# Kernel optimization log

Measured on AMD Instinct MI355X. Metric: run time of the kernel, lower is better.

Reference implementation:

```python
import jax, jax.numpy as jnp
import numpy as np

C = 256          # in_channels == out_channels
L = 131072       # sequence length (multiple of BL)
BL = 64          # dilation == sliding-attention block length
CQ = C // 2      # q/k channels (r1=2)
CV = C // 2      # v channels (r2=2)
ALPHA = 1.0
EPS_IN = 1e-5    # InstanceNorm eps


def setup_inputs() -> dict:
    key = jax.random.key(0)
    ks = jax.random.split(key, 16)
    s = 0.05
    return {
        "x": jax.random.normal(ks[0], (1, C, L), jnp.float32),
        "f": jax.random.normal(ks[1], (1, C, L), jnp.float32),
        "mask": jnp.ones((1, 1, L), jnp.float32),
        # ConvFeedForward: Conv1d(C, C, 3, padding=BL, dilation=BL)
        "Wff": jax.random.normal(ks[2], (C, C, 3), jnp.float32) * s,
        "bff": jax.random.normal(ks[3], (C,), jnp.float32) * s,
        # AttLayer 1x1 convs
        "Wq": jax.random.normal(ks[4], (CQ, C), jnp.float32) * s,
        "bq": jax.random.normal(ks[5], (CQ,), jnp.float32) * s,
        "Wk": jax.random.normal(ks[6], (CQ, C), jnp.float32) * s,
        "bk": jax.random.normal(ks[7], (CQ,), jnp.float32) * s,
        "Wv": jax.random.normal(ks[8], (CV, C), jnp.float32) * s,
        "bv": jax.random.normal(ks[9], (CV,), jnp.float32) * s,
        "Wo": jax.random.normal(ks[10], (C, CV), jnp.float32) * s,
        "bo": jax.random.normal(ks[11], (C,), jnp.float32) * s,
        # AttModule.conv_1x1
        "Wc": jax.random.normal(ks[12], (C, C), jnp.float32) * s,
        "bc": jax.random.normal(ks[13], (C,), jnp.float32) * s,
    }


def _conv1x1(W, b, x):  # x: (B, Cin, L)
    return jnp.einsum('oc,bcl->bol', W, x) + b[None, :, None]


def _forward(x, f, mask, Wff, bff, Wq, bq, Wk, bk, Wv, bv, Wo, bo, Wc, bc):
    # --- ConvFeedForward: dilated conv + ReLU (same-length output) ---
    out = jax.lax.conv_general_dilated(
        x, Wff, window_strides=(1,), padding=[(BL, BL)], rhs_dilation=(BL,),
        dimension_numbers=('NCH', 'OIH', 'NCH')) + bff[None, :, None]
    out = jax.nn.relu(out)  # (1, C, L)

    # --- InstanceNorm1d (affine=False, biased var) ---
    mu = out.mean(axis=-1, keepdims=True)
    var = out.var(axis=-1, keepdims=True)
    xn = (out - mu) * jax.lax.rsqrt(var + EPS_IN)

    # --- AttLayer (sliding_att, decoder: value from f) ---
    q = _conv1x1(Wq, bq, xn)   # (1, CQ, L)
    k = _conv1x1(Wk, bk, xn)   # (1, CQ, L)
    v = _conv1x1(Wv, bv, f)    # (1, CV, L)

    nb = L // BL
    half = BL // 2
    pm = mask[:, 0:1, :]                         # (1,1,L) padding mask
    # pad halo of BL//2 zeros on each side of k, v, padding_mask
    kp = jnp.pad(k, ((0, 0), (0, 0), (half, half)))
    vp = jnp.pad(v, ((0, 0), (0, 0), (half, half)))
    mp = jnp.pad(pm, ((0, 0), (0, 0), (half, half)))
    # window index: block i sees [i*BL, i*BL + 2*BL) of the padded sequence
    idx = jnp.arange(nb)[:, None] * BL + jnp.arange(2 * BL)[None, :]  # (nb, 2BL)
    kw = kp[:, :, idx]   # (1, CQ, nb, 2BL)
    vw = vp[:, :, idx]   # (1, CV, nb, 2BL)
    mw = mp[:, 0, idx]   # (1, nb, 2BL)

    # window mask: query i attends keys [i, i+BL) within the 2BL window
    d = jnp.arange(2 * BL)[None, :] - jnp.arange(BL)[:, None]
    wm = ((d >= 0) & (d < BL)).astype(x.dtype)          # (BL, 2BL)
    fm = wm[None, None] * mw[:, :, None, :]             # (1, nb, BL, 2BL)

    qb = q.reshape(1, CQ, nb, BL)
    energy = jnp.einsum('bcnl,bcnm->bnlm', qb, kw) / np.sqrt(CQ).astype(x.dtype)
    att = jax.nn.softmax(energy + jnp.log(fm + 1e-6), axis=-1) * fm
    ov = jnp.einsum('bcnm,bnlm->bcnl', vw, att)         # (1, CV, nb, BL)
    oo = jnp.einsum('oc,bcnl->bonl', Wo, jax.nn.relu(ov)) + bo[None, :, None, None]
    att_out = oo.reshape(1, C, L) * pm                  # (1, C, L)

    # --- scaled residual + 1x1 conv + (dropout=identity) + masked residual ---
    h = ALPHA * att_out + out
    h = _conv1x1(Wc, bc, h)
    return (x + h) * mask


def reference(x, f, mask, Wff, bff, Wq, bq, Wk, bk, Wv, bv, Wo, bo, Wc, bc):
    return _forward(x, f, mask, Wff, bff, Wq, bq, Wk, bk, Wv, bv, Wo, bo, Wc, bc)
```

## Files before the change

### kernel.cpp

```cpp
#include <hip/hip_runtime.h>

#define L_LEN 131072
#define NB    2048
#define NT    1024

typedef unsigned short u16;
typedef __attribute__((ext_vector_type(4))) float f32x4;
typedef __attribute__((ext_vector_type(8))) short s16x8;
typedef __attribute__((ext_vector_type(4))) short s16x4;

#define WS_OUTT  0ull
#define WS_QT    67108864ull
#define WS_PSUM  100663296ull
#define WS_PSQ   101711872ull
#define WS_MEAN  102760448ull
#define WS_RSTD  102761472ull
#define WS_WFFB  102762496ull
#define WS_WQKB  103155712ull
#define WS_WVB   103286784ull
#define WS_WOB   103352320ull
#define WS_WCB   103417856ull
#define WS_BQKP  103548928ull
#define WS_ZP    103549952ull

__device__ __forceinline__ u16 f2bf(float v){
  union { float f; unsigned u; } a; a.f = v;
  unsigned r = a.u + 0x7fffu + ((a.u >> 16) & 1u);
  return (u16)(r >> 16);
}
__device__ __forceinline__ float bf2f(u16 u){
  union { unsigned u; float f; } a; a.u = ((unsigned)u) << 16; return a.f;
}
__device__ __forceinline__ unsigned cvtpk(float a, float b){
  unsigned r;
  asm("v_cvt_pk_bf16_f32 %0, %1, %2" : "=v"(r) : "v"(a), "v"(b));
  return r;
}
__device__ __forceinline__ f32x4 mfma16(s16x8 a, s16x8 b, f32x4 c){
  return __builtin_amdgcn_mfma_f32_16x16x32_bf16(a, b, c, 0, 0, 0);
}
__device__ __forceinline__ s16x8 ld8(const void* p){ return *(const s16x8*)p; }
__device__ __forceinline__ void gl_lds16(const void* g, void* l){
  __builtin_amdgcn_global_load_lds(
      (const __attribute__((address_space(1))) unsigned int*)g,
      (__attribute__((address_space(3))) unsigned int*)l, 16, 0, 0);
}

__global__ __launch_bounds__(256) void k_prep(
    const float* __restrict__ Wff, const float* __restrict__ Wv,
    const float* __restrict__ Wo,  const float* __restrict__ Wc,
    short* __restrict__ wffb, short* __restrict__ wvb,
    short* __restrict__ wob,  short* __restrict__ wcb, u16* __restrict__ zp)
{
  int i = blockIdx.x * 256 + threadIdx.x;
  if (i < 196608){
    int o = i / 768, kk = i % 768;
    int t = kk >> 8, c = kk & 255;
    wffb[i] = (short)f2bf(Wff[(o*256 + c)*3 + t]);
  } else if (i < 229376){ int j = i - 196608; wvb[j] = (short)f2bf(Wv[j]); }
  else if (i < 262144){ int j = i - 229376; wob[j] = (short)f2bf(Wo[j]); }
  else if (i < 327680){ int j = i - 262144; wcb[j] = (short)f2bf(Wc[j]); }
  if (blockIdx.x == 0 && threadIdx.x < 32) zp[threadIdx.x] = 0;
}

__global__ __launch_bounds__(256) void k_xbfT(
    const float* __restrict__ x, u16* __restrict__ xbfT)
{
  __shared__ u16 t[64*264];
  const int l0 = blockIdx.x * 64, tid = threadIdx.x;
  const int chb = tid >> 4, pq = tid & 15;
  #pragma unroll
  for (int rep = 0; rep < 16; ++rep){
    const int ch = rep*16 + chb;
    const int pos0 = pq*4;
    f32x4 v = *(const f32x4*)(x + (size_t)ch*L_LEN + l0 + pos0);
    const unsigned u01 = cvtpk(v[0], v[1]), u23 = cvtpk(v[2], v[3]);
    t[(pos0+0)*264 + ch] = (u16)(u01 & 0xffffu);
    t[(pos0+1)*264 + ch] = (u16)(u01 >> 16);
    t[(pos0+2)*264 + ch] = (u16)(u23 & 0xffffu);
    t[(pos0+3)*264 + ch] = (u16)(u23 >> 16);
  }
  __syncthreads();
  #pragma unroll
  for (int rep = 0; rep < 8; ++rep){
    const int idx = rep*256 + tid;
    const int row = idx >> 5, j = idx & 31;
    s16x8 vv = ld8(&t[row*264 + 8*j]);
    *(s16x8*)(xbfT + (size_t)(l0 + row)*256 + 8*j) = vv;
  }
}

__global__ __launch_bounds__(512, 4) void k_conv(
    const float* __restrict__ xunused, const u16* __restrict__ xbfT,
    const short* __restrict__ wffb, const float* __restrict__ bff,
    const u16* __restrict__ zp, u16* __restrict__ outT,
    float* __restrict__ psum, float* __restrict__ psq)
{
  __shared__ u16 wbuf[2*256*32];
  const int bid = blockIdx.x;
  const int wg = (bid & 7) * 128 + (bid >> 3);
  const int l0 = wg * 128;
  const int tid = threadIdx.x;
  const int w = tid >> 6, lane = tid & 63, p = lane & 15, g = lane >> 4;
  const int wo = w >> 1, wp = w & 1;

  auto stage = [&](int cg, int buf){
    #pragma unroll
    for (int gi = 0; gi < 2; ++gi){
      const int rw = 32*w + 16*gi + (lane >> 2);
      const int slot = lane & 3;
      const int cb = slot ^ (((rw >> 2) ^ rw) & 3);
      const int wpos = l0 - 64 + rw;
      const u16* src = (wpos >= 0 && wpos < L_LEN)
                     ? (xbfT + (size_t)wpos*256 + cg*32 + cb*8) : zp;
      u16* dst = &wbuf[buf*8192 + (32*w + 16*gi)*32];
      gl_lds16(src, dst);
    }
  };

  stage(0, 0);
  __syncthreads();

  f32x4 acc[4][4] = {};
  #pragma unroll 1
  for (int cg = 0; cg < 8; ++cg){
    const int cur = cg & 1;
    if (cg < 7) stage(cg + 1, cur ^ 1);
    #pragma unroll
    for (int t = 0; t < 3; ++t){
      s16x8 a[4];
      #pragma unroll
      for (int fm = 0; fm < 4; ++fm)
        a[fm] = ld8(wffb + (size_t)(64*wo + 16*fm + p)*768 + t*256 + cg*32 + 8*g);
      #pragma unroll
      for (int fn = 0; fn < 4; ++fn){
        const int r = 64*t + 64*wp + 16*fn + p;
        s16x8 b = ld8(&wbuf[cur*8192 + r*32 + ((g ^ (((r >> 2) ^ r) & 3)) * 8)]);
        #pragma unroll
        for (int fm = 0; fm < 4; ++fm)
          acc[fm][fn] = mfma16(a[fm], b, acc[fm][fn]);
      }
    }
    __syncthreads();
  }

  float* sf = (float*)wbuf;
  #pragma unroll
  for (int fm = 0; fm < 4; ++fm){
    const int o0 = 64*wo + 16*fm + 4*g;
    float sv[4] = {0,0,0,0}, qv[4] = {0,0,0,0};
    #pragma unroll
    for (int fn = 0; fn < 4; ++fn){
      const int pos = 64*wp + 16*fn + p;
      s16x4 pk;
      #pragma unroll
      for (int i = 0; i < 4; ++i){
        float val = fmaxf(acc[fm][fn][i] + bff[o0 + i], 0.f);
        pk[i] = (short)f2bf(val);
        sv[i] += val; qv[i] += val*val;
      }
      *(s16x4*)(outT + (size_t)(l0 + pos)*256 + o0) = pk;
    }
    #pragma unroll
    for (int i = 0; i < 4; ++i){
      #pragma unroll
      for (int d = 1; d < 16; d <<= 1){
        sv[i] += __shfl_xor(sv[i], d, 16);
        qv[i] += __shfl_xor(qv[i], d, 16);
      }
      if (p == 0){
        sf[(wp*256 + o0 + i)*2 + 0] = sv[i];
        sf[(wp*256 + o0 + i)*2 + 1] = qv[i];
      }
    }
  }
  __syncthreads();
  if (tid < 256){
    psum[(size_t)tid*NT + wg] = sf[(0*256 + tid)*2 + 0] + sf[(1*256 + tid)*2 + 0];
    psq [(size_t)tid*NT + wg] = sf[(0*256 + tid)*2 + 1] + sf[(1*256 + tid)*2 + 1];
  }
}

__global__ __launch_bounds__(256) void k_stats(
    const float* __restrict__ psum, const float* __restrict__ psq,
    float* __restrict__ mean, float* __restrict__ rstd)
{
  __shared__ float ss[256], sq[256];
  const int ch = blockIdx.x, tid = threadIdx.x;
  float a = 0.f, b = 0.f;
  for (int j = tid; j < NT; j += 256){ a += psum[(size_t)ch*NT + j]; b += psq[(size_t)ch*NT + j]; }
  ss[tid] = a; sq[tid] = b;
  __syncthreads();
  for (int st = 128; st > 0; st >>= 1){
    if (tid < st){ ss[tid] += ss[tid+st]; sq[tid] += sq[tid+st]; }
    __syncthreads();
  }
  if (tid == 0){
    float m = ss[0] / (float)L_LEN;
    float v = sq[0] / (float)L_LEN - m*m;
    mean[ch] = m;
    rstd[ch] = rsqrtf(v + 1e-5f);
  }
}

__global__ __launch_bounds__(256) void k_adj(
    const float* __restrict__ Wq, const float* __restrict__ Wk,
    const float* __restrict__ bq, const float* __restrict__ bk,
    const float* __restrict__ mean, const float* __restrict__ rstd,
    short* __restrict__ wqkb, float* __restrict__ bqkp)
{
  __shared__ float red[256];
  const int o = blockIdx.x, c = threadIdx.x;
  const float* src = (o < 128) ? (Wq + (size_t)o*256) : (Wk + (size_t)(o-128)*256);
  const float bias = (o < 128) ? bq[o] : bk[o-128];
  float wv = src[c] * rstd[c];
  wqkb[o*256 + c] = (short)f2bf(wv);
  red[c] = wv * mean[c];
  __syncthreads();
  for (int st = 128; st > 0; st >>= 1){
    if (c < st) red[c] += red[c+st];
    __syncthreads();
  }
  if (c == 0) bqkp[o] = bias - red[0];
}

__global__ __launch_bounds__(512, 4) void k_v(
    const float* __restrict__ fin, const short* __restrict__ wvb,
    const float* __restrict__ bv, u16* __restrict__ vout)
{
  __shared__ u16 xs[2*128*40];
  const int wg = blockIdx.x, l0 = wg * 128;
  const int tid = threadIdx.x;
  const int w = tid >> 6, lane = tid & 63, p = lane & 15, g = lane >> 4;
  const int cl = tid >> 4, posq = tid & 15;

  {
    #pragma unroll
    for (int u = 0; u < 2; ++u){
      const int row = 8*posq + 4*u;
      f32x4 v = *(const f32x4*)(fin + (size_t)cl*L_LEN + l0 + row);
      const unsigned r01 = cvtpk(v[0], v[1]);
      const unsigned r23 = cvtpk(v[2], v[3]);
      xs[(row+0)*40 + (cl ^ (8*(((row+0)>>2)&3)))] = (u16)(r01 & 0xffffu);
      xs[(row+1)*40 + (cl ^ (8*(((row+1)>>2)&3)))] = (u16)(r01 >> 16);
      xs[(row+2)*40 + (cl ^ (8*(((row+2)>>2)&3)))] = (u16)(r23 & 0xffffu);
      xs[(row+3)*40 + (cl ^ (8*(((row+3)>>2)&3)))] = (u16)(r23 >> 16);
    }
  }
  __syncthreads();

  f32x4 acc[8] = {};
  #pragma unroll 1
  for (int cg = 0; cg < 8; ++cg){
    const int cur = (cg & 1) * 5120;
    const int nxt = ((cg + 1) & 1) * 5120;
    f32x4 vv[2];
    const bool have = (cg < 7);
    if (have){
      #pragma unroll
      for (int u = 0; u < 2; ++u){
        const int row = 8*posq + 4*u;
        vv[u] = *(const f32x4*)(fin + (size_t)((cg+1)*32 + cl)*L_LEN + l0 + row);
      }
    }
    s16x8 af = ld8(wvb + (size_t)(16*w + p)*256 + cg*32 + 8*g);
    #pragma unroll
    for (int fn = 0; fn < 8; ++fn){
      const int row = 16*fn + p;
      s16x8 b = ld8(&xs[cur + row*40 + ((8*g) ^ (8*((row>>2)&3)))]);
      acc[fn] = mfma16(af, b, acc[fn]);
    }
    if (have){
      #pragma unroll
      for (int u = 0; u < 2; ++u){
        const int row = 8*posq + 4*u;
        const unsigned r01 = cvtpk(vv[u][0], vv[u][1]);
        const unsigned r23 = cvtpk(vv[u][2], vv[u][3]);
        xs[nxt + (row+0)*40 + (cl ^ (8*(((row+0)>>2)&3)))] = (u16)(r01 & 0xffffu);
        xs[nxt + (row+1)*40 + (cl ^ (8*(((row+1)>>2)&3)))] = (u16)(r01 >> 16);
        xs[nxt + (row+2)*40 + (cl ^ (8*(((row+2)>>2)&3)))] = (u16)(r23 & 0xffffu);
        xs[nxt + (row+3)*40 + (cl ^ (8*(((row+3)>>2)&3)))] = (u16)(r23 >> 16);
      }
    }
    __syncthreads();
  }
  #pragma unroll
  for (int fn = 0; fn < 8; ++fn){
    #pragma unroll
    for (int i = 0; i < 4; ++i){
      const int cv = 16*w + 4*g + i;
      vout[(size_t)cv*L_LEN + l0 + 16*fn + p] = f2bf(acc[fn][i] + bv[cv]);
    }
  }
}

__global__ __launch_bounds__(512, 2) void k_qk(
    const u16* __restrict__ outT, const short* __restrict__ wqkb,
    const float* __restrict__ bqkp, u16* __restrict__ qT, u16* __restrict__ kT)
{
  extern __shared__ u16 tile[];
  const int wg = blockIdx.x, l0 = wg * 128;
  const int tid = threadIdx.x;
  const int w = tid >> 6, lane = tid & 63, p = lane & 15, g = lane >> 4;
  #pragma unroll
  for (int rep = 0; rep < 8; ++rep){
    const int idx = rep*512 + tid;
    const int r = idx >> 5, cc = idx & 31;
    s16x8 vput = ld8(outT + (size_t)(l0 + r)*256 + cc*8);
    *(s16x8*)(&tile[r*256 + ((cc*8) ^ ((r&7)<<3))]) = vput;
  }
  __syncthreads();
  f32x4 acc[2][8] = {};
  #pragma unroll
  for (int kk = 0; kk < 8; ++kk){
    s16x8 af[2];
    af[0] = ld8(wqkb + (size_t)(32*w +      p)*256 + 32*kk + 8*g);
    af[1] = ld8(wqkb + (size_t)(32*w + 16 + p)*256 + 32*kk + 8*g);
    #pragma unroll
    for (int fn = 0; fn < 8; ++fn){
      const int r = 16*fn + p;
      s16x8 b = ld8(&tile[r*256 + ((32*kk + 8*g) ^ ((r&7)<<3))]);
      acc[0][fn] = mfma16(af[0], b, acc[0][fn]);
      acc[1][fn] = mfma16(af[1], b, acc[1][fn]);
    }
  }
  #pragma unroll
  for (int fm = 0; fm < 2; ++fm){
    const int R0 = 32*w + 16*fm + 4*g;
    #pragma unroll
    for (int fn = 0; fn < 8; ++fn){
      s16x4 pk;
      #pragma unroll
      for (int i = 0; i < 4; ++i) pk[i] = (short)f2bf(acc[fm][fn][i] + bqkp[R0+i]);
      const size_t row = (size_t)(l0 + 16*fn + p);
      if (R0 < 128) *(s16x4*)(qT + row*128 + R0)       = pk;
      else          *(s16x4*)(kT + row*128 + R0 - 128) = pk;
    }
  }
}

__global__ __launch_bounds__(256, 4) void k_attn(
    const u16* __restrict__ qT, const u16* __restrict__ kT,
    const u16* __restrict__ vg, const short* __restrict__ wob,
    const float* __restrict__ bo, const float* __restrict__ mask,
    u16* __restrict__ outT)
{
  __shared__ u16 klds[16384];
  __shared__ float maskw[128];
  const int tid = threadIdx.x;
  const int w = tid >> 6, lane = tid & 63, p = lane & 15, g = lane >> 4;
  const int n = blockIdx.x, s = n * 64;
  const float SCALE = 0.08838834764831845f;

  #pragma unroll
  for (int rep = 0; rep < 8; ++rep){
    const int idx = rep*256 + tid;
    const int m = idx >> 4, cc = idx & 15;
    const int gpos = s - 32 + m;
    s16x8 vput = {};
    if (gpos >= 0 && gpos < L_LEN) vput = ld8(kT + (size_t)gpos*128 + cc*8);
    *(s16x8*)(&klds[m*128 + ((cc*8) ^ ((m&7)<<3))]) = vput;
  }
  if (tid < 128){
    const int gp = s - 32 + tid;
    maskw[tid] = (gp >= 0 && gp < L_LEN) ? mask[gp] : 0.f;
  }
  __syncthreads();

  f32x4 e[8] = {};
  #pragma unroll
  for (int kk = 0; kk < 4; ++kk){
    s16x8 aq = ld8(qT + (size_t)(s + 16*w + p)*128 + 32*kk + 8*g);
    #pragma unroll
    for (int fn = 0; fn < 8; ++fn){
      const int m = 16*fn + p;
      s16x8 b = ld8(&klds[m*128 + ((32*kk + 8*g) ^ ((m&7)<<3))]);
      e[fn] = mfma16(aq, b, e[fn]);
    }
  }
  float M[4] = {-1e30f,-1e30f,-1e30f,-1e30f};
  float S[4] = {0.f,0.f,0.f,0.f};
  #pragma unroll
  for (int fn = 0; fn < 8; ++fn){
    #pragma unroll
    for (int i = 0; i < 4; ++i){
      const int mm = 16*fn + p;
      const int l_ = 16*w + 4*g + i;
      const int d = mm - l_;
      const float fmv = (d >= 0 && d < 64) ? maskw[mm] : 0.f;
      const float z = e[fn][i]*SCALE + __logf(fmv + 1e-6f);
      e[fn][i] = z;
      M[i] = fmaxf(M[i], z);
    }
  }
  #pragma unroll
  for (int i = 0; i < 4; ++i){
    #pragma unroll
    for (int d = 1; d < 16; d <<= 1) M[i] = fmaxf(M[i], __shfl_xor(M[i], d, 16));
  }
  #pragma unroll
  for (int fn = 0; fn < 8; ++fn){
    #pragma unroll
    for (int i = 0; i < 4; ++i){
      const float pv = __expf(e[fn][i] - M[i]);
      e[fn][i] = pv;
      S[i] += pv;
    }
  }
  #pragma unroll
  for (int i = 0; i < 4; ++i){
    #pragma unroll
    for (int d = 1; d < 16; d <<= 1) S[i] += __shfl_xor(S[i], d, 16);
  }
  float rinv[4];
  #pragma unroll
  for (int i = 0; i < 4; ++i) rinv[i] = 1.f / S[i];
  __syncthreads();
  #pragma unroll
  for (int fn = 0; fn < 8; ++fn){
    #pragma unroll
    for (int i = 0; i < 4; ++i){
      const int mm = 16*fn + p;
      const int l_ = 16*w + 4*g + i;
      const int d = mm - l_;
      const float fmv = (d >= 0 && d < 64) ? maskw[mm] : 0.f;
      klds[l_*128 + (mm ^ ((l_&7)<<3))] = f2bf(e[fn][i] * rinv[i] * fmv);
    }
  }
  __syncthreads();

  f32x4 accp[2][4] = {};
  #pragma unroll
  for (int kk = 0; kk < 4; ++kk){
    int gp0 = s - 32 + 32*kk + 8*g;
    gp0 = max(0, min(gp0, L_LEN - 8));
    s16x8 a0 = ld8(vg + (size_t)(32*w +      p)*L_LEN + gp0);
    s16x8 a1 = ld8(vg + (size_t)(32*w + 16 + p)*L_LEN + gp0);
    #pragma unroll
    for (int fn = 0; fn < 4; ++fn){
      const int l_ = 16*fn + p;
      s16x8 b = ld8(&klds[l_*128 + ((32*kk + 8*g) ^ ((l_&7)<<3))]);
      accp[0][fn] = mfma16(a0, b, accp[0][fn]);
      accp[1][fn] = mfma16(a1, b, accp[1][fn]);
    }
  }
  #pragma unroll
  for (int fm = 0; fm < 2; ++fm){
    #pragma unroll
    for (int fn = 0; fn < 4; ++fn){
      const int l_ = 16*fn + p;
      s16x4 pk;
      #pragma unroll
      for (int i = 0; i < 4; ++i) pk[i] = (short)f2bf(fmaxf(accp[fm][fn][i], 0.f));
      const int cv0 = 32*w + 16*fm + 4*g;
      *(s16x4*)(&klds[8192 + l_*128 + (cv0 ^ ((l_&7)<<3))]) = pk;
    }
  }
  __syncthreads();

  f32x4 acco[4][4] = {};
  #pragma unroll
  for (int kk = 0; kk < 4; ++kk){
    s16x8 a[4];
    #pragma unroll
    for (int fm = 0; fm < 4; ++fm)
      a[fm] = ld8(wob + (size_t)(64*w + 16*fm + p)*128 + 32*kk + 8*g);
    #pragma unroll
    for (int fn = 0; fn < 4; ++fn){
      const int l_ = 16*fn + p;
      s16x8 b = ld8(&klds[8192 + l_*128 + ((32*kk + 8*g) ^ ((l_&7)<<3))]);
      #pragma unroll
      for (int fm = 0; fm < 4; ++fm) acco[fm][fn] = mfma16(a[fm], b, acco[fm][fn]);
    }
  }
  #pragma unroll
  for (int fm = 0; fm < 4; ++fm){
    const int o0 = 64*w + 16*fm + 4*g;
    #pragma unroll
    for (int fn = 0; fn < 4; ++fn){
      const int l_ = 16*fn + p;
      const float pml = maskw[32 + l_];
      u16* hp = outT + (size_t)(s + l_)*256 + o0;
      s16x4 res = *(const s16x4*)hp;
      s16x4 pk;
      #pragma unroll
      for (int i = 0; i < 4; ++i){
        float hv = (acco[fm][fn][i] + bo[o0+i]) * pml + bf2f((u16)res[i]);
        pk[i] = (short)f2bf(hv);
      }
      *(s16x4*)hp = pk;
    }
  }
}

__global__ __launch_bounds__(512, 2) void k_wc(
    const u16* __restrict__ hT, const short* __restrict__ wcb,
    const float* __restrict__ bc, const float* __restrict__ x,
    const float* __restrict__ mask, float* __restrict__ dout)
{
  extern __shared__ u16 tile[];
  const int wg = blockIdx.x, l0 = wg * 128;
  const int tid = threadIdx.x;
  const int w = tid >> 6, lane = tid & 63, p = lane & 15, g = lane >> 4;
  #pragma unroll
  for (int rep = 0; rep < 8; ++rep){
    const int idx = rep*512 + tid;
    const int r = idx >> 5, cc = idx & 31;
    s16x8 vput = ld8(hT + (size_t)(l0 + r)*256 + cc*8);
    *(s16x8*)(&tile[r*256 + ((cc*8) ^ ((r&7)<<3))]) = vput;
  }
  __syncthreads();
  f32x4 acc[2][8] = {};
  #pragma unroll
  for (int kk = 0; kk < 8; ++kk){
    s16x8 af[2];
    af[0] = ld8(wcb + (size_t)(32*w +      p)*256 + 32*kk + 8*g);
    af[1] = ld8(wcb + (size_t)(32*w + 16 + p)*256 + 32*kk + 8*g);
    #pragma unroll
    for (int fn = 0; fn < 8; ++fn){
      const int r = 16*fn + p;
      s16x8 b = ld8(&tile[r*256 + ((32*kk + 8*g) ^ ((r&7)<<3))]);
      acc[0][fn] = mfma16(af[0], b, acc[0][fn]);
      acc[1][fn] = mfma16(af[1], b, acc[1][fn]);
    }
  }
  #pragma unroll
  for (int fm = 0; fm < 2; ++fm){
    const int o0 = 32*w + 16*fm + 4*g;
    #pragma unroll
    for (int fn = 0; fn < 8; ++fn){
      const int pos = l0 + 16*fn + p;
      const float mk = mask[pos];
      #pragma unroll
      for (int i = 0; i < 4; ++i){
        const size_t idx = (size_t)(o0+i)*L_LEN + pos;
        dout[idx] = (x[idx] + acc[fm][fn][i] + bc[o0+i]) * mk;
      }
    }
  }
}

extern "C" void kernel_launch(void* const* d_in, const int* in_sizes, int n_in,
                              void* d_out, int out_size, void* d_ws, size_t ws_size,
                              hipStream_t stream)
{
  (void)in_sizes; (void)n_in; (void)out_size; (void)ws_size;
  const float* x    = (const float*)d_in[0];
  const float* f    = (const float*)d_in[1];
  const float* mask = (const float*)d_in[2];
  const float* Wff  = (const float*)d_in[3];
  const float* bff  = (const float*)d_in[4];
  const float* Wq   = (const float*)d_in[5];
  const float* bq   = (const float*)d_in[6];
  const float* Wk   = (const float*)d_in[7];
  const float* bk   = (const float*)d_in[8];
  const float* Wv   = (const float*)d_in[9];
  const float* bv   = (const float*)d_in[10];
  const float* Wo   = (const float*)d_in[11];
  const float* bo   = (const float*)d_in[12];
  const float* Wc   = (const float*)d_in[13];
  const float* bc   = (const float*)d_in[14];

  char* ws = (char*)d_ws;
  u16*   outT = (u16*)(ws + WS_OUTT);
  u16*   qT   = (u16*)(ws + WS_QT);
  float* psum = (float*)(ws + WS_PSUM);
  float* psq  = (float*)(ws + WS_PSQ);
  float* mean = (float*)(ws + WS_MEAN);
  float* rstd = (float*)(ws + WS_RSTD);
  short* wffb = (short*)(ws + WS_WFFB);
  short* wqkb = (short*)(ws + WS_WQKB);
  short* wvb  = (short*)(ws + WS_WVB);
  short* wob  = (short*)(ws + WS_WOB);
  short* wcb  = (short*)(ws + WS_WCB);
  float* bqkp = (float*)(ws + WS_BQKP);
  u16*   zp   = (u16*)(ws + WS_ZP);

  u16* vbuf = (u16*)d_out;
  u16* ktb  = (u16*)((char*)d_out + 33554432);
  u16* xbfT = (u16*)((char*)d_out + 67108864);

  (void)hipFuncSetAttribute((const void*)k_qk,
                            hipFuncAttributeMaxDynamicSharedMemorySize, 65536);
  (void)hipFuncSetAttribute((const void*)k_wc,
                            hipFuncAttributeMaxDynamicSharedMemorySize, 65536);

  k_prep <<<1280, 256, 0, stream>>>(Wff, Wv, Wo, Wc, wffb, wvb, wob, wcb, zp);
  k_xbfT <<<2048, 256, 0, stream>>>(x, xbfT);
  k_conv <<<NT,   512, 0, stream>>>(x, xbfT, wffb, bff, zp, outT, psum, psq);
  k_stats<<<256,  256, 0, stream>>>(psum, psq, mean, rstd);
  k_adj  <<<256,  256, 0, stream>>>(Wq, Wk, bq, bk, mean, rstd, wqkb, bqkp);
  k_v    <<<NT,   512, 0, stream>>>(f, wvb, bv, vbuf);
  k_qk   <<<NT,   512, 65536, stream>>>(outT, wqkb, bqkp, qT, ktb);
  k_attn <<<NB,   256, 0, stream>>>(qT, ktb, vbuf, wob, bo, mask, outT);
  k_wc   <<<NT,   512, 65536, stream>>>(outT, wcb, bc, x, mask, (float*)d_out);
}
```

Baseline: 415.2 us.

## Retile dilated conv: split output channels across blocks, stage weights in LDS

The conv kernel now launches twice as many 256-thread blocks, each computing a 128-output-channel by 128-position tile instead of the full 256 channels. Both the weight tile and the shifted input window are staged into LDS through a 24-step double-buffered K loop over taps and channel groups, replacing the per-lane global loads of weights. The aim is better occupancy and load balance, plus cheaper operand fetches. In exchange each input window is loaded twice, once per channel half, and there are more barriers.

```diff
diff --git a/kernel.cpp b/kernel.cpp
--- a/kernel.cpp
+++ b/kernel.cpp
@@ -90,31 +90,40 @@
   }
 }
 
-__global__ __launch_bounds__(512, 4) void k_conv(
-    const float* __restrict__ xunused, const u16* __restrict__ xbfT,
-    const short* __restrict__ wffb, const float* __restrict__ bff,
-    const u16* __restrict__ zp, u16* __restrict__ outT,
-    float* __restrict__ psum, float* __restrict__ psq)
-{
-  __shared__ u16 wbuf[2*256*32];
+__global__ __launch_bounds__(256, 4) void k_conv(
+    const u16* __restrict__ xbfT, const short* __restrict__ wffb,
+    const float* __restrict__ bff, const u16* __restrict__ zp,
+    u16* __restrict__ outT, float* __restrict__ psum, float* __restrict__ psq)
+{
+  __shared__ u16 sm[16384];
   const int bid = blockIdx.x;
-  const int wg = (bid & 7) * 128 + (bid >> 3);
-  const int l0 = wg * 128;
+  const int swz = (bid & 7) * 256 + (bid >> 3);
+  const int oh = swz & 1, pt = swz >> 1;
+  const int l0 = pt * 128;
   const int tid = threadIdx.x;
   const int w = tid >> 6, lane = tid & 63, p = lane & 15, g = lane >> 4;
-  const int wo = w >> 1, wp = w & 1;
-
-  auto stage = [&](int cg, int buf){
+  const int wm = w >> 1, wn = w & 1;
+
+  auto fsw = [](int r){ return ((r >> 2) ^ r) & 3; };
+
+  auto stage = [&](int ks, int buf){
+    const int t = ks >> 3, c0 = (ks & 7) * 32;
     #pragma unroll
     for (int gi = 0; gi < 2; ++gi){
-      const int rw = 32*w + 16*gi + (lane >> 2);
+      const int r = 32*w + 16*gi + (lane >> 2);
       const int slot = lane & 3;
-      const int cb = slot ^ (((rw >> 2) ^ rw) & 3);
-      const int wpos = l0 - 64 + rw;
-      const u16* src = (wpos >= 0 && wpos < L_LEN)
-                     ? (xbfT + (size_t)wpos*256 + cg*32 + cb*8) : zp;
-      u16* dst = &wbuf[buf*8192 + (32*w + 16*gi)*32];
-      gl_lds16(src, dst);
+      const int cb = (slot ^ fsw(r)) * 8;
+      {
+        const short* srcA = wffb + (size_t)(128*oh + r)*768 + t*256 + c0 + cb;
+        gl_lds16(srcA, &sm[buf*8192 + (32*w + 16*gi)*32]);
+      }
+      {
+        const int wpos = l0 + 64*t - 64 + r;
+        const u16* srcB = (wpos >= 0 && wpos < L_LEN)
+                        ? (xbfT + (size_t)wpos*256 + c0 + cb)
+                        : (zp + (lane & 3)*8);
+        gl_lds16(srcB, &sm[buf*8192 + 4096 + (32*w + 16*gi)*32]);
+      }
     }
   };
 
@@ -123,43 +132,45 @@
 
   f32x4 acc[4][4] = {};
   #pragma unroll 1
-  for (int cg = 0; cg < 8; ++cg){
-    const int cur = cg & 1;
-    if (cg < 7) stage(cg + 1, cur ^ 1);
-    #pragma unroll
-    for (int t = 0; t < 3; ++t){
-      s16x8 a[4];
-      #pragma unroll
-      for (int fm = 0; fm < 4; ++fm)
-        a[fm] = ld8(wffb + (size_t)(64*wo + 16*fm + p)*768 + t*256 + cg*32 + 8*g);
-      #pragma unroll
-      for (int fn = 0; fn < 4; ++fn){
-        const int r = 64*t + 64*wp + 16*fn + p;
-        s16x8 b = ld8(&wbuf[cur*8192 + r*32 + ((g ^ (((r >> 2) ^ r) & 3)) * 8)]);
-        #pragma unroll
-        for (int fm = 0; fm < 4; ++fm)
-          acc[fm][fn] = mfma16(a[fm], b, acc[fm][fn]);
-      }
+  for (int ks = 0; ks < 24; ++ks){
+    const int cur = ks & 1;
+    if (ks < 23) stage(ks + 1, cur ^ 1);
+    s16x8 a[4], b[4];
+    #pragma unroll
+    for (int fm = 0; fm < 4; ++fm){
+      const int r = 64*wm + 16*fm + p;
+      a[fm] = ld8(&sm[cur*8192 + r*32 + ((g ^ fsw(r)) * 8)]);
+    }
+    #pragma unroll
+    for (int fn = 0; fn < 4; ++fn){
+      const int r = 64*wn + 16*fn + p;
+      b[fn] = ld8(&sm[cur*8192 + 4096 + r*32 + ((g ^ fsw(r)) * 8)]);
+    }
+    #pragma unroll
+    for (int fm = 0; fm < 4; ++fm){
+      #pragma unroll
+      for (int fn = 0; fn < 4; ++fn)
+        acc[fm][fn] = mfma16(a[fm], b[fn], acc[fm][fn]);
     }
     __syncthreads();
   }
 
-  float* sf = (float*)wbuf;
+  float* sf = (float*)sm;
   #pragma unroll
   for (int fm = 0; fm < 4; ++fm){
-    const int o0 = 64*wo + 16*fm + 4*g;
+    const int ol = 64*wm + 16*fm + 4*g;
     float sv[4] = {0,0,0,0}, qv[4] = {0,0,0,0};
     #pragma unroll
     for (int fn = 0; fn < 4; ++fn){
-      const int pos = 64*wp + 16*fn + p;
+      const int pos = l0 + 64*wn + 16*fn + p;
       s16x4 pk;
       #pragma unroll
       for (int i = 0; i < 4; ++i){
-        float val = fmaxf(acc[fm][fn][i] + bff[o0 + i], 0.f);
+        float val = fmaxf(acc[fm][fn][i] + bff[128*oh + ol + i], 0.f);
         pk[i] = (short)f2bf(val);
         sv[i] += val; qv[i] += val*val;
       }
-      *(s16x4*)(outT + (size_t)(l0 + pos)*256 + o0) = pk;
+      *(s16x4*)(outT + (size_t)pos*256 + 128*oh + ol) = pk;
     }
     #pragma unroll
     for (int i = 0; i < 4; ++i){
@@ -168,16 +179,19 @@
         sv[i] += __shfl_xor(sv[i], d, 16);
         qv[i] += __shfl_xor(qv[i], d, 16);
       }
-      if (p == 0){
-        sf[(wp*256 + o0 + i)*2 + 0] = sv[i];
-        sf[(wp*256 + o0 + i)*2 + 1] = qv[i];
-      }
-    }
-  }
-  __syncthreads();
-  if (tid < 256){
-    psum[(size_t)tid*NT + wg] = sf[(0*256 + tid)*2 + 0] + sf[(1*256 + tid)*2 + 0];
-    psq [(size_t)tid*NT + wg] = sf[(0*256 + tid)*2 + 1] + sf[(1*256 + tid)*2 + 1];
+    }
+    if (p == 0){
+      #pragma unroll
+      for (int i = 0; i < 4; ++i){
+        sf[(wn*128 + ol + i)*2 + 0] = sv[i];
+        sf[(wn*128 + ol + i)*2 + 1] = qv[i];
+      }
+    }
+  }
+  __syncthreads();
+  if (tid < 128){
+    psum[(size_t)(128*oh + tid)*NT + pt] = sf[(0 + tid)*2 + 0] + sf[(128 + tid)*2 + 0];
+    psq [(size_t)(128*oh + tid)*NT + pt] = sf[(0 + tid)*2 + 1] + sf[(128 + tid)*2 + 1];
   }
 }
 
@@ -587,7 +601,7 @@
 
   k_prep <<<1280, 256, 0, stream>>>(Wff, Wv, Wo, Wc, wffb, wvb, wob, wcb, zp);
   k_xbfT <<<2048, 256, 0, stream>>>(x, xbfT);
-  k_conv <<<NT,   512, 0, stream>>>(x, xbfT, wffb, bff, zp, outT, psum, psq);
+  k_conv <<<2048, 256, 0, stream>>>(xbfT, wffb, bff, zp, outT, psum, psq);
   k_stats<<<256,  256, 0, stream>>>(psum, psq, mean, rstd);
   k_adj  <<<256,  256, 0, stream>>>(Wq, Wk, bq, bk, mean, rstd, wqkb, bqkp);
   k_v    <<<NT,   512, 0, stream>>>(f, wvb, bv, vbuf);
```

Measured after the change: 376.8 us. -9.2%, faster.
